# Optimization experiments

Hardware: AMD Instinct MI355X
Metric: run time of the kernel (lower is better)

The kernel has to match this reference:

```python
import jax, jax.numpy as jnp
import numpy as np

SEQ_LEN = 128   # sourceL == seq_len
BATCH   = 256
E_DIM   = 512
H_DIM   = 512
C_EXPL  = 10.0  # tanh_exploration


def setup_inputs() -> dict:
    key = jax.random.key(0)
    ks = jax.random.split(key, 24)
    rn = lambda k, shape, s=0.05: (jax.random.normal(k, shape, jnp.float32) * s)
    inp = {
        'decoder_input':  rn(ks[0], (BATCH, E_DIM), 1.0),
        'embedded_inputs': rn(ks[1], (SEQ_LEN, BATCH, E_DIM), 1.0),
        'h0': rn(ks[2], (BATCH, H_DIM), 1.0),
        'c0': rn(ks[3], (BATCH, H_DIM), 1.0),
        'context': rn(ks[4], (SEQ_LEN, BATCH, H_DIM), 1.0),
        # LSTM cell weights (nn.Linear: y = x @ W.T + b)
        'Wi': rn(ks[5], (4 * H_DIM, E_DIM)), 'bi': rn(ks[6], (4 * H_DIM,)),
        'Wh': rn(ks[7], (4 * H_DIM, H_DIM)), 'bh': rn(ks[8], (4 * H_DIM,)),
        # glimpse attention (use_tanh=False)
        'g_Wq': rn(ks[9], (H_DIM, H_DIM)),  'g_bq': rn(ks[10], (H_DIM,)),
        'g_Wref': rn(ks[11], (H_DIM, H_DIM)), 'g_bref': rn(ks[12], (H_DIM,)),
        'g_v': rn(ks[13], (H_DIM,), 1.0 / np.sqrt(H_DIM)),
        # pointer attention (use_tanh=True, C=10)
        'p_Wq': rn(ks[14], (H_DIM, H_DIM)),  'p_bq': rn(ks[15], (H_DIM,)),
        'p_Wref': rn(ks[16], (H_DIM, H_DIM)), 'p_bref': rn(ks[17], (H_DIM,)),
        'p_v': rn(ks[18], (H_DIM,), 1.0 / np.sqrt(H_DIM)),
    }
    return inp


def reference(decoder_input, embedded_inputs, h0, c0, context,
              Wi, bi, Wh, bh,
              g_Wq, g_bq, g_Wref, g_bref, g_v,
              p_Wq, p_bq, p_Wref, p_bref, p_v):
    L, B, H = context.shape

    # Conv1d(k=1) on ref is loop-invariant: precompute e = W_ref @ context, [B,H,L]
    e_g = jnp.einsum('oh,lbh->bol', g_Wref, context) + g_bref[None, :, None]
    e_p = jnp.einsum('oh,lbh->bol', p_Wref, context) + p_bref[None, :, None]
    barange = jnp.arange(B)

    def step(carry, key):
        hx, cx, dec_in, mask, prev = carry
        # fused LSTM cell
        gates = dec_in @ Wi.T + bi + hx @ Wh.T + bh
        i_, f_, g_, o_ = jnp.split(gates, 4, axis=1)
        cy = jax.nn.sigmoid(f_) * cx + jax.nn.sigmoid(i_) * jnp.tanh(g_)
        hy = jax.nn.sigmoid(o_) * jnp.tanh(cy)
        # mark previously selected index as visited
        mask = mask.at[barange, prev].set(True)
        # glimpse (n_glimpses=1, use_tanh=False)
        q = hy @ g_Wq.T + g_bq                                   # [B,H]
        u = jnp.einsum('h,bhl->bl', g_v, jnp.tanh(q[:, :, None] + e_g))
        u = jnp.where(mask, -jnp.inf, u)
        g_l = jnp.einsum('bhl,bl->bh', e_g, jax.nn.softmax(u, axis=1))
        # pointer (use_tanh=True): logits = C * tanh(u), then mask
        q = g_l @ p_Wq.T + p_bq
        u = jnp.einsum('h,bhl->bl', p_v, jnp.tanh(q[:, :, None] + e_p))
        u = jnp.where(mask, -jnp.inf, C_EXPL * jnp.tanh(u))
        probs = jax.nn.softmax(u, axis=1)                        # [B,L]
        # stochastic decode: multinomial sample, gather next embedding
        idxs = jax.random.categorical(key, u, axis=1)            # [B]
        dec_next = embedded_inputs[idxs, barange, :]             # [B,E]
        return (hy, cy, dec_next, mask, idxs), (probs, idxs)

    mask0 = jnp.zeros((B, L), dtype=bool).at[:, 0].set(True)
    prev0 = jnp.zeros((B,), dtype=jnp.int32)
    keys = jax.random.split(jax.random.key(1), L - 1)
    (hy, cy, _, _, _), (probs_seq, idxs_seq) = jax.lax.scan(
        step, (h0, c0, decoder_input, mask0, prev0), keys)

    prob_0 = jnp.zeros((B, L), jnp.float32).at[:, 0].set(1.0)
    outputs = jnp.concatenate([prob_0[None], probs_seq], axis=0)          # [L,B,L]
    selections = jnp.concatenate([prev0[None], idxs_seq], axis=0)         # [L,B]
    return outputs, selections, hy, cy
```

## Files before the change

kernel.cpp:

```cpp
#include <hip/hip_runtime.h>
#include <stdint.h>

#ifndef THREEFRY_PARTITIONABLE
#define THREEFRY_PARTITIONABLE 1
#endif

#define LSEQ 128
#define BSZ  256
#define HD   512
#define G4   2048

#define SEL_OFF  ((size_t)LSEQ * BSZ * LSEQ)
#define HY_OFF   (SEL_OFF + (size_t)LSEQ * BSZ)
#define CY_OFF   (HY_OFF + (size_t)BSZ * HD)

__device__ __forceinline__ uint32_t rotl_(uint32_t v, int r) { return (v << r) | (v >> (32 - r)); }

__device__ __forceinline__ void tf2x32(uint32_t k0, uint32_t k1,
                                       uint32_t x0, uint32_t x1,
                                       uint32_t &o0, uint32_t &o1)
{
  uint32_t k2 = k0 ^ k1 ^ 0x1BD11BDAu;
  x0 += k0; x1 += k1;
#define TFR(r) { x0 += x1; x1 = rotl_(x1,(r)); x1 ^= x0; }
  TFR(13) TFR(15) TFR(26) TFR(6)
  x0 += k1; x1 += k2 + 1u;
  TFR(17) TFR(29) TFR(16) TFR(24)
  x0 += k2; x1 += k0 + 2u;
  TFR(13) TFR(15) TFR(26) TFR(6)
  x0 += k0; x1 += k1 + 3u;
  TFR(17) TFR(29) TFR(16) TFR(24)
  x0 += k1; x1 += k2 + 4u;
  TFR(13) TFR(15) TFR(26) TFR(6)
  x0 += k2; x1 += k0 + 5u;
#undef TFR
  o0 = x0; o1 = x1;
}

__device__ __forceinline__ void step_key(int t, uint32_t &kA, uint32_t &kB)
{
#if THREEFRY_PARTITIONABLE
  uint32_t o0, o1;
  tf2x32(0u, 1u, 0u, (uint32_t)t, o0, o1);
  kA = o0; kB = o1;
#else
  uint32_t o0, o1;
  uint32_t j = 2u * (uint32_t)t;
  if (j < 127u) { tf2x32(0u, 1u, j, 127u + j, o0, o1); kA = o0; }
  else          { tf2x32(0u, 1u, j - 127u, j, o0, o1); kA = o1; }
  j = 2u * (uint32_t)t + 1u;
  if (j < 127u) { tf2x32(0u, 1u, j, 127u + j, o0, o1); kB = o0; }
  else          { tf2x32(0u, 1u, j - 127u, j, o0, o1); kB = o1; }
#endif
}

__device__ __forceinline__ uint32_t draw_bits(uint32_t kA, uint32_t kB, uint32_t n)
{
  uint32_t y0, y1;
#if THREEFRY_PARTITIONABLE
  tf2x32(kA, kB, 0u, n, y0, y1);
  return y0 ^ y1;
#else
  uint32_t i0 = (n < 16384u) ? n : n - 16384u;
  tf2x32(kA, kB, i0, i0 + 16384u, y0, y1);
  return (n < 16384u) ? y0 : y1;
#endif
}

__device__ __forceinline__ double tanh_c(double x)
{
  float xf = (float)x;
  float ax = fabsf(xf);
  float z  = fminf(ax * 2.8853900817779268f, 50.0f);
  float e  = __builtin_amdgcn_exp2f(z);
  float d  = e + 1.0f;
  float r0 = __builtin_amdgcn_rcpf(d);
  float r  = fmaf(fmaf(-d, r0, 1.0f), r0, r0);
  float t  = copysignf(fmaf(-2.0f, r, 1.0f), xf);
  float dx = (float)(x - (double)xf);
  return (double)t + (double)((1.0f - t * t) * dx);
}

template<int RM, int CHUNK>
__global__ __launch_bounds__(256)
void gemm32(const float* __restrict__ A0, const float* __restrict__ A1, int lda,
            const float* __restrict__ B0, const float* __restrict__ B1, int ldb,
            const float* __restrict__ bias,
            double* __restrict__ Cd0, double* __restrict__ Cd1,
            float* __restrict__ Cf0, float* __restrict__ Cf1,
            int N, int K, int out_mode)
{
  constexpr int BM = RM * 16;
  constexpr int BN = 64;
  constexpr int BK = 32;
  __shared__ float As[BK][BM];
  __shared__ float Bs[BK][BN];
  const int tid = threadIdx.x;
  const int tx = tid & 15, ty = tid >> 4;
  const int z = blockIdx.z;
  const float* A = z ? A1 : A0;
  const float* B = z ? B1 : B0;
  const int m0 = blockIdx.x * BM;
  const int n0 = blockIdx.y * BN;

  const int b_r = tid >> 2, b_kq = (tid & 3) * 8;
  const int a_r  = (RM == 4) ? (tid >> 2) : (tid >> 3);
  const int a_kq = (RM == 4) ? ((tid & 3) * 8) : ((tid & 7) * 4);

  double acc[RM][4];
  float  c32[RM][4];
#pragma unroll
  for (int i = 0; i < RM; ++i)
#pragma unroll
    for (int j = 0; j < 4; ++j) { acc[i][j] = 0.0; c32[i][j] = 0.0f; }

  const float* bp0 = B + (size_t)(n0 + b_r) * ldb + b_kq;
  float4 w0 = *(const float4*)bp0;
  float4 w1 = *(const float4*)(bp0 + 4);
  const float* ap0 = A + (size_t)(m0 + a_r) * lda + a_kq;
  float4 u0 = *(const float4*)ap0;
  float4 u1 = (RM == 4) ? *(const float4*)(ap0 + 4) : u0;

  for (int k0 = 0; k0 < K; k0 += BK) {
    __syncthreads();
    Bs[b_kq + 0][b_r] = w0.x; Bs[b_kq + 1][b_r] = w0.y;
    Bs[b_kq + 2][b_r] = w0.z; Bs[b_kq + 3][b_r] = w0.w;
    Bs[b_kq + 4][b_r] = w1.x; Bs[b_kq + 5][b_r] = w1.y;
    Bs[b_kq + 6][b_r] = w1.z; Bs[b_kq + 7][b_r] = w1.w;
    As[a_kq + 0][a_r] = u0.x; As[a_kq + 1][a_r] = u0.y;
    As[a_kq + 2][a_r] = u0.z; As[a_kq + 3][a_r] = u0.w;
    if (RM == 4) {
      As[a_kq + 4][a_r] = u1.x; As[a_kq + 5][a_r] = u1.y;
      As[a_kq + 6][a_r] = u1.z; As[a_kq + 7][a_r] = u1.w;
    }
    __syncthreads();

    float4 nw0 = w0, nw1 = w1, nu0 = u0, nu1 = u1;
    if (k0 + BK < K) {
      const float* bp = B + (size_t)(n0 + b_r) * ldb + (k0 + BK) + b_kq;
      nw0 = *(const float4*)bp;
      nw1 = *(const float4*)(bp + 4);
      const float* ap = A + (size_t)(m0 + a_r) * lda + (k0 + BK) + a_kq;
      nu0 = *(const float4*)ap;
      if (RM == 4) nu1 = *(const float4*)(ap + 4);
    }

#pragma unroll
    for (int kk = 0; kk < BK; ++kk) {
      float a[RM];
      if (RM == 4) {
        float4 av = *(const float4*)&As[kk][4 * ty];
        a[0] = av.x; a[1] = av.y; a[2] = av.z; a[3] = av.w;
      } else {
        float2 av = *(const float2*)&As[kk][2 * ty];
        a[0] = av.x; a[1] = av.y;
      }
      float4 bv = *(const float4*)&Bs[kk][4 * tx];
#pragma unroll
      for (int i = 0; i < RM; ++i) {
        c32[i][0] = fmaf(a[i], bv.x, c32[i][0]);
        c32[i][1] = fmaf(a[i], bv.y, c32[i][1]);
        c32[i][2] = fmaf(a[i], bv.z, c32[i][2]);
        c32[i][3] = fmaf(a[i], bv.w, c32[i][3]);
      }
      if ((kk & (CHUNK - 1)) == (CHUNK - 1)) {
#pragma unroll
        for (int i = 0; i < RM; ++i)
#pragma unroll
          for (int j = 0; j < 4; ++j) { acc[i][j] += (double)c32[i][j]; c32[i][j] = 0.0f; }
      }
    }
    w0 = nw0; w1 = nw1; u0 = nu0; u1 = nu1;
  }

#pragma unroll
  for (int i = 0; i < RM; ++i) {
    int m = m0 + RM * ty + i;
#pragma unroll
    for (int j = 0; j < 4; ++j) {
      int n = n0 + 4 * tx + j;
      double v = acc[i][j] + (bias ? (double)bias[n] : 0.0);
      if (out_mode == 0) {
        double* Cd = z ? Cd1 : Cd0;
        Cd[(size_t)m * N + n] = v;
      } else if (out_mode == 1) {
        Cf0[(((size_t)(m & 255)) * LSEQ + (m >> 8)) * HD + n] = (float)v;
      } else if (out_mode == 2) {
        Cf0[(size_t)m * N + n] = (float)v;
      } else if (out_mode == 3) {
        Cf0[(((size_t)(m & 255)) * HD + n) * LSEQ + (m >> 8)] = (float)v;
      } else {
        float* Cf = z ? Cf1 : Cf0;
        Cf[(size_t)m * N + n] = (float)v;
      }
    }
  }
}

__global__ __launch_bounds__(256)
void transpose512(const float* __restrict__ W, float* __restrict__ WT)
{
  __shared__ float tile[32][33];
  int bx = blockIdx.x * 32, by = blockIdx.y * 32;
  int x = threadIdx.x & 31, y = threadIdx.x >> 5;
#pragma unroll
  for (int j = 0; j < 32; j += 8)
    tile[y + j][x] = W[(size_t)(by + y + j) * HD + bx + x];
  __syncthreads();
#pragma unroll
  for (int j = 0; j < 32; j += 8)
    WT[(size_t)(bx + y + j) * HD + by + x] = tile[x][y + j];
}

#define SCOMP(A0_, A1_, A2_, A3_, V4, IT)                         \
  {                                                               \
    const int h_ = (IT) * 16 + hh;                                \
    double xq_ = qs[h_];                                          \
    double vv_ = (double)vs[h_];                                  \
    A0_ += vv_ * tanh_c(xq_ + (double)(V4).x);                    \
    A1_ += vv_ * tanh_c(xq_ + (double)(V4).y);                    \
    A2_ += vv_ * tanh_c(xq_ + (double)(V4).z);                    \
    A3_ += vv_ * tanh_c(xq_ + (double)(V4).w);                    \
  }

__global__ __launch_bounds__(512)
void step_fused(const float* __restrict__ g0, const float* __restrict__ g1,
                const float* __restrict__ bi, const float* __restrict__ bh,
                const double* __restrict__ c_in, double* __restrict__ c_out,
                float* __restrict__ h_out,
                const float* __restrict__ WqT, const float* __restrict__ g_bq,
                const float* __restrict__ e_g,
                const float* __restrict__ pWqT, const float* __restrict__ p_bq,
                const float* __restrict__ e_p,
                const float* __restrict__ g_v, const float* __restrict__ p_v,
                unsigned char* __restrict__ mask,
                const float* __restrict__ emb, float* __restrict__ dec_in,
                float* __restrict__ out, int t)
{
  const int b   = blockIdx.x;
  const int tid = threadIdx.x;
  const int l   = tid & 127;
  const int lg  = tid & 31;
  const int hh  = tid >> 5;
  __shared__ float  hs[HD];
  __shared__ double qs[HD];
  __shared__ float  vs[HD];
  __shared__ double part[16][LSEQ];
  __shared__ double gls[HD];
  __shared__ double sarr[LSEQ];
  __shared__ double red[4];
  __shared__ double wv[2];
  __shared__ int    wi[2];
  __shared__ int    selidx;

  const float* egbase = e_g + (size_t)b * (HD * LSEQ) + hh * LSEQ + lg * 4;
  const float* epbase = e_p + (size_t)b * (HD * LSEQ) + hh * LSEQ + lg * 4;

  float4 B0[8], B1[8];
#pragma unroll
  for (int j = 0; j < 8; ++j)
    B0[j] = *(const float4*)(egbase + (size_t)j * (16 * LSEQ));

  {
    const int u = tid;
    const size_t base = (size_t)b * G4;
    double gi = (double)g0[base + u]        + (double)g1[base + u]        + (double)bi[u]        + (double)bh[u];
    double gf = (double)g0[base + u + 512]  + (double)g1[base + u + 512]  + (double)bi[u + 512]  + (double)bh[u + 512];
    double gg = (double)g0[base + u + 1024] + (double)g1[base + u + 1024] + (double)bi[u + 1024] + (double)bh[u + 1024];
    double go = (double)g0[base + u + 1536] + (double)g1[base + u + 1536] + (double)bi[u + 1536] + (double)bh[u + 1536];
    double si = 1.0 / (1.0 + exp(-gi));
    double sf = 1.0 / (1.0 + exp(-gf));
    double so = 1.0 / (1.0 + exp(-go));
    double cy = sf * c_in[(size_t)b * HD + u] + si * tanh(gg);
    double hy = so * tanh(cy);
    c_out[(size_t)b * HD + u] = cy;
    float hyf = (float)hy;
    h_out[(size_t)b * HD + u] = hyf;
    hs[u] = hyf;
  }
  __syncthreads();

  {
    const int h = tid;
    const float* wcol = WqT + h;
    float wA[32], wB[32];
    double a = 0.0;
#pragma unroll
    for (int j = 0; j < 32; ++j) wA[j] = wcol[(size_t)j * HD];
#pragma unroll
    for (int pair = 0; pair < 8; ++pair) {
      const int kA = pair * 64;
#pragma unroll
      for (int j = 0; j < 32; ++j) wB[j] = wcol[(size_t)(kA + 32 + j) * HD];
#pragma unroll
      for (int c = 0; c < 4; ++c) {
        float c32 = 0.0f;
#pragma unroll
        for (int j = 0; j < 8; ++j)
          c32 = fmaf(hs[kA + c * 8 + j], wA[c * 8 + j], c32);
        a += (double)c32;
      }
      if (pair < 7) {
#pragma unroll
        for (int j = 0; j < 32; ++j) wA[j] = wcol[(size_t)(kA + 64 + j) * HD];
      }
#pragma unroll
      for (int c = 0; c < 4; ++c) {
        float c32 = 0.0f;
#pragma unroll
        for (int j = 0; j < 8; ++j)
          c32 = fmaf(hs[kA + 32 + c * 8 + j], wB[c * 8 + j], c32);
        a += (double)c32;
      }
    }
    qs[tid] = a + (double)g_bq[tid];
    vs[tid] = g_v[tid];
  }
  __syncthreads();

  {
    double a0 = 0, a1 = 0, a2 = 0, a3 = 0;
#pragma unroll
    for (int j = 0; j < 8; ++j)
      B1[j] = *(const float4*)(egbase + (size_t)(8 + j) * (16 * LSEQ));
#pragma unroll
    for (int j = 0; j < 8; ++j) SCOMP(a0, a1, a2, a3, B0[j], j);
#pragma unroll
    for (int j = 0; j < 8; ++j)
      B0[j] = *(const float4*)(egbase + (size_t)(16 + j) * (16 * LSEQ));
#pragma unroll
    for (int j = 0; j < 8; ++j) SCOMP(a0, a1, a2, a3, B1[j], 8 + j);
#pragma unroll
    for (int j = 0; j < 8; ++j)
      B1[j] = *(const float4*)(egbase + (size_t)(24 + j) * (16 * LSEQ));
#pragma unroll
    for (int j = 0; j < 8; ++j) SCOMP(a0, a1, a2, a3, B0[j], 16 + j);
#pragma unroll
    for (int j = 0; j < 8; ++j) SCOMP(a0, a1, a2, a3, B1[j], 24 + j);
    part[hh][lg * 4 + 0] = a0;
    part[hh][lg * 4 + 1] = a1;
    part[hh][lg * 4 + 2] = a2;
    part[hh][lg * 4 + 3] = a3;
  }
  __syncthreads();

  bool   msk = false;
  double u = 0.0, pe = 0.0;
  if (tid < 128) {
    msk = mask[(size_t)b * LSEQ + l] != 0;
    u = 0.0;
#pragma unroll
    for (int o = 0; o < 16; ++o) u += part[o][l];
    if (msk) u = -__builtin_inf();
    double mx = u;
    for (int off = 32; off; off >>= 1) mx = fmax(mx, __shfl_xor(mx, off));
    if ((tid & 63) == 0) red[tid >> 6] = mx;
  }
  __syncthreads();
  if (tid < 128) {
    double mx = fmax(red[0], red[1]);
    pe = msk ? 0.0 : exp(u - mx);
    double sm = pe;
    for (int off = 32; off; off >>= 1) sm += __shfl_xor(sm, off);
    if ((tid & 63) == 0) red[2 + (tid >> 6)] = sm;
  }
  __syncthreads();
  if (tid < 128) sarr[l] = pe / (red[2] + red[3]);
  __syncthreads();

  {
#pragma unroll
    for (int j = 0; j < 8; ++j)
      B0[j] = *(const float4*)(epbase + (size_t)j * (16 * LSEQ));

    const float4* row = (const float4*)(e_g + ((size_t)b * HD + tid) * LSEQ);
    float4 rA[4], rB[4];
    double a = 0.0;
#pragma unroll
    for (int j = 0; j < 4; ++j) rA[j] = row[j];
#pragma unroll
    for (int r = 0; r < 4; ++r) {
#pragma unroll
      for (int j = 0; j < 4; ++j) rB[j] = row[r * 8 + 4 + j];
#pragma unroll
      for (int j = 0; j < 4; ++j) {
        int l4 = (r * 8 + j) * 4;
        float4 v = rA[j];
        a += (double)v.x * sarr[l4 + 0];
        a += (double)v.y * sarr[l4 + 1];
        a += (double)v.z * sarr[l4 + 2];
        a += (double)v.w * sarr[l4 + 3];
      }
      if (r < 3) {
#pragma unroll
        for (int j = 0; j < 4; ++j) rA[j] = row[r * 8 + 8 + j];
      }
#pragma unroll
      for (int j = 0; j < 4; ++j) {
        int l4 = (r * 8 + 4 + j) * 4;
        float4 v = rB[j];
        a += (double)v.x * sarr[l4 + 0];
        a += (double)v.y * sarr[l4 + 1];
        a += (double)v.z * sarr[l4 + 2];
        a += (double)v.w * sarr[l4 + 3];
      }
    }
    gls[tid] = a;
  }
  __syncthreads();

  {
    const float* wcol = pWqT + tid;
    float wA[32], wB[32];
    double a = 0.0;
#pragma unroll
    for (int j = 0; j < 32; ++j) wA[j] = wcol[(size_t)j * HD];
#pragma unroll
    for (int pair = 0; pair < 8; ++pair) {
      const int hA = pair * 64;
#pragma unroll
      for (int j = 0; j < 32; ++j) wB[j] = wcol[(size_t)(hA + 32 + j) * HD];
#pragma unroll
      for (int j = 0; j < 32; ++j) a += gls[hA + j] * (double)wA[j];
      if (pair < 7) {
#pragma unroll
        for (int j = 0; j < 32; ++j) wA[j] = wcol[(size_t)(hA + 64 + j) * HD];
      }
#pragma unroll
      for (int j = 0; j < 32; ++j) a += gls[hA + 32 + j] * (double)wB[j];
    }
    qs[tid] = a + (double)p_bq[tid];
    vs[tid] = p_v[tid];
  }
  __syncthreads();

  {
    double a0 = 0, a1 = 0, a2 = 0, a3 = 0;
#pragma unroll
    for (int j = 0; j < 8; ++j)
      B1[j] = *(const float4*)(epbase + (size_t)(8 + j) * (16 * LSEQ));
#pragma unroll
    for (int j = 0; j < 8; ++j) SCOMP(a0, a1, a2, a3, B0[j], j);
#pragma unroll
    for (int j = 0; j < 8; ++j)
      B0[j] = *(const float4*)(epbase + (size_t)(16 + j) * (16 * LSEQ));
#pragma unroll
    for (int j = 0; j < 8; ++j) SCOMP(a0, a1, a2, a3, B1[j], 8 + j);
#pragma unroll
    for (int j = 0; j < 8; ++j)
      B1[j] = *(const float4*)(epbase + (size_t)(24 + j) * (16 * LSEQ));
#pragma unroll
    for (int j = 0; j < 8; ++j) SCOMP(a0, a1, a2, a3, B0[j], 16 + j);
#pragma unroll
    for (int j = 0; j < 8; ++j) SCOMP(a0, a1, a2, a3, B1[j], 24 + j);
    part[hh][lg * 4 + 0] = a0;
    part[hh][lg * 4 + 1] = a1;
    part[hh][lg * 4 + 2] = a2;
    part[hh][lg * 4 + 3] = a3;
  }
  __syncthreads();

  double logit = 0.0, cand = 0.0;
  int idx = l;
  if (tid < 128) {
    double acc2 = 0.0;
#pragma unroll
    for (int o = 0; o < 16; ++o) acc2 += part[o][l];
    logit = msk ? -__builtin_inf() : 10.0 * tanh(acc2);
    double mx = logit;
    for (int off = 32; off; off >>= 1) mx = fmax(mx, __shfl_xor(mx, off));
    if ((tid & 63) == 0) red[tid >> 6] = mx;
  }
  __syncthreads();
  if (tid < 128) {
    double mx = fmax(red[0], red[1]);
    double pe2 = msk ? 0.0 : exp(logit - mx);
    double sm = pe2;
    for (int off = 32; off; off >>= 1) sm += __shfl_xor(sm, off);
    if ((tid & 63) == 0) red[2 + (tid >> 6)] = sm;
    __threadfence_block();
  }
  __syncthreads();
  if (tid < 128) {
    double mx = fmax(red[0], red[1]);
    double pe2 = msk ? 0.0 : exp(logit - mx);
    out[(size_t)(t + 1) * BSZ * LSEQ + (size_t)b * LSEQ + l] = (float)(pe2 / (red[2] + red[3]));

    uint32_t kA, kB;
    step_key(t, kA, kB);
    uint32_t bits = draw_bits(kA, kB, (uint32_t)(b * LSEQ + l));
    float f = __uint_as_float((bits >> 9) | 0x3f800000u) - 1.0f;
    const float TINY = 1.17549435e-38f;
    float uu = fmaxf(f * (1.0f - TINY) + TINY, TINY);
    float gmb = -logf(-logf(uu));
    cand = msk ? -__builtin_inf() : (logit + (double)gmb);

    for (int off = 32; off; off >>= 1) {
      double c2 = __shfl_xor(cand, off);
      int    i2 = __shfl_xor(idx, off);
      if (c2 > cand || (c2 == cand && i2 < idx)) { cand = c2; idx = i2; }
    }
    if ((tid & 63) == 0) { wv[tid >> 6] = cand; wi[tid >> 6] = idx; }
  }
  __syncthreads();
  if (tid == 0) {
    double c2 = wv[1]; int i2 = wi[1];
    if (c2 > cand || (c2 == cand && i2 < idx)) { cand = c2; idx = i2; }
    selidx = idx;
    out[SEL_OFF + (size_t)(t + 1) * BSZ + b] = (float)idx;
    mask[(size_t)b * LSEQ + idx] = 1;
  }
  __syncthreads();
  {
    int sidx = selidx;
    dec_in[(size_t)b * HD + tid] = emb[((size_t)sidx * BSZ + b) * HD + tid];
  }
}

__global__ __launch_bounds__(256)
void init_kernel(const float* __restrict__ dec0, const float* __restrict__ h0,
                 const float* __restrict__ c0, float* __restrict__ dec_in,
                 float* __restrict__ hf, double* __restrict__ c,
                 unsigned char* __restrict__ mask, float* __restrict__ out)
{
  int i = blockIdx.x * blockDim.x + threadIdx.x;
  if (i < BSZ * HD) { hf[i] = h0[i]; c[i] = (double)c0[i]; dec_in[i] = dec0[i]; }
  if (i < BSZ * LSEQ) {
    mask[i] = ((i & (LSEQ - 1)) == 0) ? 1 : 0;
    out[i] = ((i & (LSEQ - 1)) == 0) ? 1.0f : 0.0f;
  }
  if (i < BSZ) out[SEL_OFF + i] = 0.0f;
}

__global__ __launch_bounds__(256)
void finalize(const float* __restrict__ hf, const double* __restrict__ c,
              float* __restrict__ out)
{
  int i = blockIdx.x * blockDim.x + threadIdx.x;
  if (i < BSZ * HD) {
    out[HY_OFF + i] = hf[i];
    out[CY_OFF + i] = (float)c[i];
  }
}

extern "C" void kernel_launch(void* const* d_in, const int* in_sizes, int n_in,
                              void* d_out, int out_size, void* d_ws, size_t ws_size,
                              hipStream_t stream)
{
  (void)in_sizes; (void)n_in; (void)out_size; (void)ws_size;
  const float* dec0  = (const float*)d_in[0];
  const float* emb   = (const float*)d_in[1];
  const float* h0    = (const float*)d_in[2];
  const float* c0    = (const float*)d_in[3];
  const float* ctx   = (const float*)d_in[4];
  const float* Wi    = (const float*)d_in[5];
  const float* bi    = (const float*)d_in[6];
  const float* Wh    = (const float*)d_in[7];
  const float* bh    = (const float*)d_in[8];
  const float* gWq   = (const float*)d_in[9];
  const float* gbq   = (const float*)d_in[10];
  const float* gWref = (const float*)d_in[11];
  const float* gbref = (const float*)d_in[12];
  const float* gv    = (const float*)d_in[13];
  const float* pWq   = (const float*)d_in[14];
  const float* pbq   = (const float*)d_in[15];
  const float* pWref = (const float*)d_in[16];
  const float* pbref = (const float*)d_in[17];
  const float* pv    = (const float*)d_in[18];
  float* out = (float*)d_out;

  char* ws = (char*)d_ws;
  size_t off = 0;
  auto take = [&](size_t bytes) -> char* {
    char* p = ws + off;
    off += (bytes + 255) & ~(size_t)255;
    return p;
  };
  float*  e_g   = (float*) take((size_t)BSZ * LSEQ * HD * 4);
  float*  e_p   = (float*) take((size_t)BSZ * LSEQ * HD * 4);
  float*  g0f   = (float*) take((size_t)BSZ * G4 * 4);
  float*  g1f   = (float*) take((size_t)BSZ * G4 * 4);
  double* cb0   = (double*)take((size_t)BSZ * HD * 8);
  double* cb1   = (double*)take((size_t)BSZ * HD * 8);
  float*  hf0   = (float*) take((size_t)BSZ * HD * 4);
  float*  hf1   = (float*) take((size_t)BSZ * HD * 4);
  float*  WqT   = (float*) take((size_t)HD * HD * 4);
  float*  pWqT  = (float*) take((size_t)HD * HD * 4);
  float*  decb  = (float*) take((size_t)BSZ * HD * 4);
  unsigned char* mask = (unsigned char*)take((size_t)BSZ * LSEQ);

  init_kernel<<<512, 256, 0, stream>>>(dec0, h0, c0, decb, hf0, cb0, mask, out);
  transpose512<<<dim3(16, 16), 256, 0, stream>>>(gWq, WqT);
  transpose512<<<dim3(16, 16), 256, 0, stream>>>(pWq, pWqT);

  gemm32<4, 8><<<dim3(BSZ * LSEQ / 64, HD / 64, 1), 256, 0, stream>>>(
      ctx, nullptr, HD, gWref, nullptr, HD, gbref,
      nullptr, nullptr, e_g, nullptr, HD, HD, 3);
  gemm32<4, 8><<<dim3(BSZ * LSEQ / 64, HD / 64, 1), 256, 0, stream>>>(
      ctx, nullptr, HD, pWref, nullptr, HD, pbref,
      nullptr, nullptr, e_p, nullptr, HD, HD, 3);

  double* cb[2] = { cb0, cb1 };
  float*  hf[2] = { hf0, hf1 };
  for (int t = 0; t < LSEQ - 1; ++t) {
    int rs = t & 1, wsl = rs ^ 1;
    gemm32<4, 8><<<dim3(BSZ / 64, G4 / 64, 2), 256, 0, stream>>>(
        decb, hf[rs], HD, Wi, Wh, HD, nullptr,
        nullptr, nullptr, g0f, g1f, G4, HD, 4);
    step_fused<<<BSZ, 512, 0, stream>>>(g0f, g1f, bi, bh,
                                        cb[rs], cb[wsl], hf[wsl],
                                        WqT, gbq, e_g, pWqT, pbq, e_p, gv, pv,
                                        mask, emb, decb, out, t);
  }
  finalize<<<BSZ * HD / 256, 256, 0, stream>>>(hf[1], cb[1], out);
}
```

Before: 13.70 ms.

## Use float tanh in attention scoring and retile GEMM to 512 threads

Replaces the double-input tanh with its first-order correction by a pure float tanh, so the query plus key sum is formed in float inside the attention scoring loop. The GEMM is retiled to 512 threads per 64x64 tile, each thread computing a 4x2 output block, which raises per-block parallelism and lowers register use per thread. A redundant block-level thread fence in the softmax reduction is also dropped. The float sums lose some precision relative to the double path, which could shift sampled indices in borderline cases.

```diff
diff --git a/kernel.cpp b/kernel.cpp
--- a/kernel.cpp
+++ b/kernel.cpp
@@ -67,22 +67,19 @@
 #endif
 }
 
-__device__ __forceinline__ double tanh_c(double x)
-{
-  float xf = (float)x;
+__device__ __forceinline__ float tanh_f(float xf)
+{
   float ax = fabsf(xf);
   float z  = fminf(ax * 2.8853900817779268f, 50.0f);
   float e  = __builtin_amdgcn_exp2f(z);
   float d  = e + 1.0f;
   float r0 = __builtin_amdgcn_rcpf(d);
   float r  = fmaf(fmaf(-d, r0, 1.0f), r0, r0);
-  float t  = copysignf(fmaf(-2.0f, r, 1.0f), xf);
-  float dx = (float)(x - (double)xf);
-  return (double)t + (double)((1.0f - t * t) * dx);
-}
-
-template<int RM, int CHUNK>
-__global__ __launch_bounds__(256)
+  return copysignf(fmaf(-2.0f, r, 1.0f), xf);
+}
+
+template<int CHUNK>
+__global__ __launch_bounds__(512)
 void gemm32(const float* __restrict__ A0, const float* __restrict__ A1, int lda,
             const float* __restrict__ B0, const float* __restrict__ B1, int ldb,
             const float* __restrict__ bias,
@@ -90,95 +87,73 @@
             float* __restrict__ Cf0, float* __restrict__ Cf1,
             int N, int K, int out_mode)
 {
-  constexpr int BM = RM * 16;
+  constexpr int BM = 64;
   constexpr int BN = 64;
   constexpr int BK = 32;
   __shared__ float As[BK][BM];
   __shared__ float Bs[BK][BN];
   const int tid = threadIdx.x;
-  const int tx = tid & 15, ty = tid >> 4;
+  const int tx = tid & 31, ty = tid >> 5;
   const int z = blockIdx.z;
   const float* A = z ? A1 : A0;
   const float* B = z ? B1 : B0;
   const int m0 = blockIdx.x * BM;
   const int n0 = blockIdx.y * BN;
 
-  const int b_r = tid >> 2, b_kq = (tid & 3) * 8;
-  const int a_r  = (RM == 4) ? (tid >> 2) : (tid >> 3);
-  const int a_kq = (RM == 4) ? ((tid & 3) * 8) : ((tid & 7) * 4);
-
-  double acc[RM][4];
-  float  c32[RM][4];
-#pragma unroll
-  for (int i = 0; i < RM; ++i)
-#pragma unroll
-    for (int j = 0; j < 4; ++j) { acc[i][j] = 0.0; c32[i][j] = 0.0f; }
-
-  const float* bp0 = B + (size_t)(n0 + b_r) * ldb + b_kq;
+  const int r_ = tid >> 3, kq = (tid & 7) * 4;
+
+  double acc[4][2];
+  float  c32[4][2];
+#pragma unroll
+  for (int i = 0; i < 4; ++i)
+#pragma unroll
+    for (int j = 0; j < 2; ++j) { acc[i][j] = 0.0; c32[i][j] = 0.0f; }
+
+  const float* bp0 = B + (size_t)(n0 + r_) * ldb + kq;
   float4 w0 = *(const float4*)bp0;
-  float4 w1 = *(const float4*)(bp0 + 4);
-  const float* ap0 = A + (size_t)(m0 + a_r) * lda + a_kq;
+  const float* ap0 = A + (size_t)(m0 + r_) * lda + kq;
   float4 u0 = *(const float4*)ap0;
-  float4 u1 = (RM == 4) ? *(const float4*)(ap0 + 4) : u0;
 
   for (int k0 = 0; k0 < K; k0 += BK) {
     __syncthreads();
-    Bs[b_kq + 0][b_r] = w0.x; Bs[b_kq + 1][b_r] = w0.y;
-    Bs[b_kq + 2][b_r] = w0.z; Bs[b_kq + 3][b_r] = w0.w;
-    Bs[b_kq + 4][b_r] = w1.x; Bs[b_kq + 5][b_r] = w1.y;
-    Bs[b_kq + 6][b_r] = w1.z; Bs[b_kq + 7][b_r] = w1.w;
-    As[a_kq + 0][a_r] = u0.x; As[a_kq + 1][a_r] = u0.y;
-    As[a_kq + 2][a_r] = u0.z; As[a_kq + 3][a_r] = u0.w;
-    if (RM == 4) {
-      As[a_kq + 4][a_r] = u1.x; As[a_kq + 5][a_r] = u1.y;
-      As[a_kq + 6][a_r] = u1.z; As[a_kq + 7][a_r] = u1.w;
-    }
+    Bs[kq + 0][r_] = w0.x; Bs[kq + 1][r_] = w0.y;
+    Bs[kq + 2][r_] = w0.z; Bs[kq + 3][r_] = w0.w;
+    As[kq + 0][r_] = u0.x; As[kq + 1][r_] = u0.y;
+    As[kq + 2][r_] = u0.z; As[kq + 3][r_] = u0.w;
     __syncthreads();
 
-    float4 nw0 = w0, nw1 = w1, nu0 = u0, nu1 = u1;
+    float4 nw0 = w0, nu0 = u0;
     if (k0 + BK < K) {
-      const float* bp = B + (size_t)(n0 + b_r) * ldb + (k0 + BK) + b_kq;
-      nw0 = *(const float4*)bp;
-      nw1 = *(const float4*)(bp + 4);
-      const float* ap = A + (size_t)(m0 + a_r) * lda + (k0 + BK) + a_kq;
-      nu0 = *(const float4*)ap;
-      if (RM == 4) nu1 = *(const float4*)(ap + 4);
+      nw0 = *(const float4*)(B + (size_t)(n0 + r_) * ldb + (k0 + BK) + kq);
+      nu0 = *(const float4*)(A + (size_t)(m0 + r_) * lda + (k0 + BK) + kq);
     }
 
 #pragma unroll
     for (int kk = 0; kk < BK; ++kk) {
-      float a[RM];
-      if (RM == 4) {
-        float4 av = *(const float4*)&As[kk][4 * ty];
-        a[0] = av.x; a[1] = av.y; a[2] = av.z; a[3] = av.w;
-      } else {
-        float2 av = *(const float2*)&As[kk][2 * ty];
-        a[0] = av.x; a[1] = av.y;
-      }
-      float4 bv = *(const float4*)&Bs[kk][4 * tx];
-#pragma unroll
-      for (int i = 0; i < RM; ++i) {
+      float4 av = *(const float4*)&As[kk][4 * ty];
+      float2 bv = *(const float2*)&Bs[kk][2 * tx];
+      float a[4] = { av.x, av.y, av.z, av.w };
+#pragma unroll
+      for (int i = 0; i < 4; ++i) {
         c32[i][0] = fmaf(a[i], bv.x, c32[i][0]);
         c32[i][1] = fmaf(a[i], bv.y, c32[i][1]);
-        c32[i][2] = fmaf(a[i], bv.z, c32[i][2]);
-        c32[i][3] = fmaf(a[i], bv.w, c32[i][3]);
       }
       if ((kk & (CHUNK - 1)) == (CHUNK - 1)) {
 #pragma unroll
-        for (int i = 0; i < RM; ++i)
-#pragma unroll
-          for (int j = 0; j < 4; ++j) { acc[i][j] += (double)c32[i][j]; c32[i][j] = 0.0f; }
-      }
-    }
-    w0 = nw0; w1 = nw1; u0 = nu0; u1 = nu1;
-  }
-
-#pragma unroll
-  for (int i = 0; i < RM; ++i) {
-    int m = m0 + RM * ty + i;
-#pragma unroll
-    for (int j = 0; j < 4; ++j) {
-      int n = n0 + 4 * tx + j;
+        for (int i = 0; i < 4; ++i)
+#pragma unroll
+          for (int j = 0; j < 2; ++j) { acc[i][j] += (double)c32[i][j]; c32[i][j] = 0.0f; }
+      }
+    }
+    w0 = nw0; u0 = nu0;
+  }
+
+#pragma unroll
+  for (int i = 0; i < 4; ++i) {
+    int m = m0 + 4 * ty + i;
+#pragma unroll
+    for (int j = 0; j < 2; ++j) {
+      int n = n0 + 2 * tx + j;
       double v = acc[i][j] + (bias ? (double)bias[n] : 0.0);
       if (out_mode == 0) {
         double* Cd = z ? Cd1 : Cd0;
@@ -215,12 +190,12 @@
 #define SCOMP(A0_, A1_, A2_, A3_, V4, IT)                         \
   {                                                               \
     const int h_ = (IT) * 16 + hh;                                \
-    double xq_ = qs[h_];                                          \
-    double vv_ = (double)vs[h_];                                  \
-    A0_ += vv_ * tanh_c(xq_ + (double)(V4).x);                    \
-    A1_ += vv_ * tanh_c(xq_ + (double)(V4).y);                    \
-    A2_ += vv_ * tanh_c(xq_ + (double)(V4).z);                    \
-    A3_ += vv_ * tanh_c(xq_ + (double)(V4).w);                    \
+    const float  xq_ = (float)qs[h_];                             \
+    const double vv_ = (double)vs[h_];                            \
+    A0_ += vv_ * (double)tanh_f(xq_ + (V4).x);                    \
+    A1_ += vv_ * (double)tanh_f(xq_ + (V4).y);                    \
+    A2_ += vv_ * (double)tanh_f(xq_ + (V4).z);                    \
+    A3_ += vv_ * (double)tanh_f(xq_ + (V4).w);                    \
   }
 
 __global__ __launch_bounds__(512)
@@ -478,7 +453,6 @@
     double sm = pe2;
     for (int off = 32; off; off >>= 1) sm += __shfl_xor(sm, off);
     if ((tid & 63) == 0) red[2 + (tid >> 6)] = sm;
-    __threadfence_block();
   }
   __syncthreads();
   if (tid < 128) {
@@ -593,10 +567,10 @@
   transpose512<<<dim3(16, 16), 256, 0, stream>>>(gWq, WqT);
   transpose512<<<dim3(16, 16), 256, 0, stream>>>(pWq, pWqT);
 
-  gemm32<4, 8><<<dim3(BSZ * LSEQ / 64, HD / 64, 1), 256, 0, stream>>>(
+  gemm32<8><<<dim3(BSZ * LSEQ / 64, HD / 64, 1), 512, 0, stream>>>(
       ctx, nullptr, HD, gWref, nullptr, HD, gbref,
       nullptr, nullptr, e_g, nullptr, HD, HD, 3);
-  gemm32<4, 8><<<dim3(BSZ * LSEQ / 64, HD / 64, 1), 256, 0, stream>>>(
+  gemm32<8><<<dim3(BSZ * LSEQ / 64, HD / 64, 1), 512, 0, stream>>>(
       ctx, nullptr, HD, pWref, nullptr, HD, pbref,
       nullptr, nullptr, e_p, nullptr, HD, HD, 3);
 
@@ -604,7 +578,7 @@
   float*  hf[2] = { hf0, hf1 };
   for (int t = 0; t < LSEQ - 1; ++t) {
     int rs = t & 1, wsl = rs ^ 1;
-    gemm32<4, 8><<<dim3(BSZ / 64, G4 / 64, 2), 256, 0, stream>>>(
+    gemm32<8><<<dim3(BSZ / 64, G4 / 64, 2), 512, 0, stream>>>(
         decb, hf[rs], HD, Wi, Wh, HD, nullptr,
         nullptr, nullptr, g0f, g1f, G4, HD, 4);
     step_fused<<<BSZ, 512, 0, stream>>>(g0f, g1f, bi, bh,
```

Result: faster. 13.03 ms, median of 2 (-4.9%).
